# Kernel optimization log

Hardware: AMD Instinct MI355X
Metric: run time of the kernel (lower is better)

Reference implementation:

```python
import jax, jax.numpy as jnp
import numpy as np

B, L, E = 4, 2048, 1024
H, D = 16, 64  # heads, head_dim; H*D == E


def setup_inputs() -> dict:
    key = jax.random.key(0)
    ks = jax.random.split(key, 6)
    s = 0.02
    return {
        "x": jax.random.normal(ks[0], (B, L, E), dtype=jnp.float32),
        "Wq": jax.random.normal(ks[1], (E, H * D), dtype=jnp.float32) * s,
        "Wk": jax.random.normal(ks[2], (E, H * D), dtype=jnp.float32) * s,
        "Wv": jax.random.normal(ks[3], (E, H * D), dtype=jnp.float32) * s,
        "Wo": jax.random.normal(ks[4], (H * D, E), dtype=jnp.float32) * s,
        "bo": jax.random.normal(ks[5], (E,), dtype=jnp.float32) * s,
    }


def reference(x, Wq, Wk, Wv, Wo, bo):
    b, l, e = x.shape
    q = (x @ Wq).reshape(b, l, H, D)
    k = (x @ Wk).reshape(b, l, H, D)
    v = (x @ Wv).reshape(b, l, H, D)
    # NOTE: original scales by sqrt(embed_size), not sqrt(head_dim)
    energy = jnp.einsum('nqhd,nkhd->nhqk', q, k)
    attn = jax.nn.softmax(energy / jnp.sqrt(jnp.float32(e)), axis=3)
    out = jnp.einsum('nhql,nlhd->nqhd', attn, v).reshape(b, l, H * D)
    return out @ Wo + bo
```

## Files before the change

kernel.cpp:

```cpp
#include <hip/hip_runtime.h>

#define B_ 4
#define L_ 2048
#define E_ 1024
#define H_ 16
#define D_ 64
#define CSCALE 0.045084960222629414f

typedef short s16x8 __attribute__((ext_vector_type(8)));
typedef short s16x4 __attribute__((ext_vector_type(4)));
typedef float f32x4 __attribute__((ext_vector_type(4)));

__device__ __forceinline__ unsigned short f2bf(float f) {
  union { float f; unsigned int u; } v;
  v.f = f;
  unsigned int u = v.u;
  u += 0x7fffu + ((u >> 16) & 1u);
  return (unsigned short)(u >> 16);
}

__device__ __forceinline__ void async16(const void* g, void* l) {
  __builtin_amdgcn_global_load_lds(
      (__attribute__((address_space(1))) void*)(g),
      (__attribute__((address_space(3))) void*)(l), 16, 0, 0);
}

__global__ void k_prep(const float* __restrict__ x,
                       const float* __restrict__ Wq, const float* __restrict__ Wk,
                       const float* __restrict__ Wv, const float* __restrict__ Wo,
                       unsigned short* __restrict__ xb,
                       unsigned short* __restrict__ Wt, unsigned short* __restrict__ WoT) {
  __shared__ float t[32][33];
  int bid = blockIdx.x, tid = threadIdx.x;
  if (bid < 8192) {
    int i = bid * 256 + tid;
    float4 v = ((const float4*)x)[i];
    ushort4 o;
    o.x = f2bf(v.x); o.y = f2bf(v.y); o.z = f2bf(v.z); o.w = f2bf(v.w);
    ((ushort4*)xb)[i] = o;
    return;
  }
  int tt = bid - 8192;
  int wsel = tt >> 10, tile = tt & 1023;
  const float* in = (wsel == 0) ? Wq : (wsel == 1) ? Wk : (wsel == 2) ? Wv : Wo;
  unsigned short* out = (wsel == 0) ? Wt : (wsel == 1) ? Wt + (1u << 20)
                        : (wsel == 2) ? Wt + (2u << 20) : WoT;
  int bx = tile & 31, by = tile >> 5;
  int tx = tid & 31, ty = tid >> 5;
  int xcol = bx * 32 + tx;
  int y0 = by * 32;
#pragma unroll
  for (int i = 0; i < 4; ++i)
    t[ty + i * 8][tx] = in[(size_t)(y0 + ty + i * 8) * 1024 + xcol];
  __syncthreads();
  int xo = by * 32 + tx;
  int yo0 = bx * 32;
#pragma unroll
  for (int i = 0; i < 4; ++i)
    out[(size_t)(yo0 + ty + i * 8) * 1024 + xo] = f2bf(t[tx][ty + i * 8]);
}

__global__ __launch_bounds__(256) void k_gemm_qkvt(
    const unsigned short* __restrict__ xb, const unsigned short* __restrict__ Wt,
    unsigned short* __restrict__ Qb, unsigned short* __restrict__ Kb,
    unsigned short* __restrict__ Vt) {
  __shared__ __align__(16) unsigned short As[128 * 32];
  __shared__ __align__(16) unsigned short Bs[128 * 32];
  const int bid = blockIdx.x;
  const int tid = threadIdx.x;
  const int w = tid >> 6, lane = tid & 63;
  const int quad = lane >> 4, mrow = lane & 15;
  const bool isQK = bid < 1024;
  int m0, n0;
  const unsigned short *PA, *PB;
  if (isQK) {
    m0 = (bid & 63) * 128;
    n0 = (bid >> 6) * 128;
    PA = xb + (size_t)m0 * 1024;
    PB = Wt + (size_t)n0 * 1024;
  } else {
    int g = bid - 1024;
    m0 = (g & 7) * 128;
    n0 = (g >> 3) * 128;
    PA = Wt + (2u << 20) + (size_t)m0 * 1024;
    PB = xb + (size_t)n0 * 1024;
  }
  const int wr = (w >> 1) * 64, wc = (w & 1) * 64;
  const f32x4 fz = {0.f, 0.f, 0.f, 0.f};
  f32x4 acc[4][4];
#pragma unroll
  for (int a = 0; a < 4; ++a)
#pragma unroll
    for (int b = 0; b < 4; ++b) acc[a][b] = fz;

  for (int kt = 0; kt < 32; ++kt) {
    __syncthreads();
#pragma unroll
    for (int r = 0; r < 2; ++r) {
      int c = r * 256 + tid;
      int row = c >> 2, cc = c & 3;
      async16(PA + (size_t)row * 1024 + kt * 32 + cc * 8, &As[c * 8]);
    }
#pragma unroll
    for (int r = 0; r < 2; ++r) {
      int c = r * 256 + tid;
      int row = c >> 2, cc = c & 3;
      async16(PB + (size_t)row * 1024 + kt * 32 + cc * 8, &Bs[c * 8]);
    }
    __syncthreads();
    s16x8 a[4], b[4];
#pragma unroll
    for (int mt = 0; mt < 4; ++mt)
      a[mt] = *(const s16x8*)&As[(wr + mt * 16 + mrow) * 32 + quad * 8];
#pragma unroll
    for (int nt = 0; nt < 4; ++nt)
      b[nt] = *(const s16x8*)&Bs[(wc + nt * 16 + mrow) * 32 + quad * 8];
#pragma unroll
    for (int mt = 0; mt < 4; ++mt)
#pragma unroll
      for (int nt = 0; nt < 4; ++nt)
        acc[mt][nt] = __builtin_amdgcn_mfma_f32_16x16x32_bf16(a[mt], b[nt], acc[mt][nt], 0, 0, 0);
  }
  if (isQK) {
#pragma unroll
    for (int mt = 0; mt < 4; ++mt)
#pragma unroll
      for (int nt = 0; nt < 4; ++nt)
#pragma unroll
        for (int i = 0; i < 4; ++i) {
          int row = m0 + wr + mt * 16 + quad * 4 + i;
          int col = n0 + wc + nt * 16 + mrow;
          int bb = row >> 11, l = row & 2047;
          if (col < 1024) {
            int h = col >> 6, d = col & 63;
            Qb[(((size_t)(bb * 16 + h)) * 2048 + l) * 64 + d] = f2bf(acc[mt][nt][i]);
          } else {
            int c2 = col - 1024, h = c2 >> 6, d = c2 & 63;
            Kb[(((size_t)(bb * 16 + h)) * 2048 + l) * 64 + d] = f2bf(acc[mt][nt][i] * CSCALE);
          }
        }
  } else {
#pragma unroll
    for (int mt = 0; mt < 4; ++mt)
#pragma unroll
      for (int nt = 0; nt < 4; ++nt)
#pragma unroll
        for (int i = 0; i < 4; ++i) {
          int f = m0 + wr + mt * 16 + quad * 4 + i;
          int tk = n0 + wc + nt * 16 + mrow;
          int bb = tk >> 11, l = tk & 2047;
          Vt[((size_t)(bb * 1024 + f)) * 2048 + l] = f2bf(acc[mt][nt][i]);
        }
  }
}

__global__ __launch_bounds__(256, 4) void k_attn(
    const unsigned short* __restrict__ Qb, const unsigned short* __restrict__ Kb,
    const unsigned short* __restrict__ Vt, unsigned short* __restrict__ AO) {
  __shared__ __align__(16) unsigned short KVs[2][8192];
  const int tid = threadIdx.x, w = tid >> 6, lane = tid & 63;
  const int quad = lane >> 4, mrow = lane & 15;
  const int bh = blockIdx.y;
  const int q0 = blockIdx.x * 128;
  const unsigned short* Qh = Qb + (size_t)bh * 2048 * 64;
  const unsigned short* Kh = Kb + (size_t)bh * 2048 * 64;
  const unsigned short* Vh = Vt + (size_t)bh * 64 * 2048;
  unsigned short* KVf = &KVs[0][0];

#pragma unroll
  for (int r = 0; r < 4; ++r) {
    int c = r * 256 + tid;
    int row = c >> 3, cl = c & 7;
    int gc = cl ^ (row & 7);
    async16(Qh + (size_t)(q0 + row) * 64 + gc * 8, &KVf[c * 8]);
  }
  __syncthreads();
  s16x8 qb[2][2];
#pragma unroll
  for (int nt = 0; nt < 2; ++nt)
#pragma unroll
    for (int ks = 0; ks < 2; ++ks) {
      int row = w * 32 + nt * 16 + mrow;
      qb[nt][ks] = *(const s16x8*)&KVf[row * 64 + (((ks * 4 + quad) ^ (row & 7)) << 3)];
    }
  __syncthreads();

#pragma unroll
  for (int r = 0; r < 2; ++r) {
    int c = r * 256 + tid;
    int row = c >> 3, cl = c & 7;
    int gc = cl ^ (row & 7);
    async16(Kh + (size_t)row * 64 + gc * 8, &KVs[0][c * 8]);
    async16(Vh + (size_t)row * 2048 + gc * 8, &KVs[0][4096 + c * 8]);
  }

  const f32x4 fz = {0.f, 0.f, 0.f, 0.f};
  f32x4 o[2][4];
  float lr[2];
#pragma unroll
  for (int nt = 0; nt < 2; ++nt) {
    lr[nt] = 0.f;
#pragma unroll
    for (int dt = 0; dt < 4; ++dt) o[nt][dt] = fz;
  }

  for (int j = 0; j < 32; ++j) {
    __syncthreads();
    const unsigned short* Kt = &KVs[j & 1][0];
    const unsigned short* Vs = &KVs[j & 1][4096];

    if (j + 1 < 32) {
      unsigned short* nb = &KVs[(j + 1) & 1][0];
#pragma unroll
      for (int r = 0; r < 2; ++r) {
        int c = r * 256 + tid;
        int row = c >> 3, cl = c & 7;
        int gc = cl ^ (row & 7);
        async16(Kh + (size_t)((j + 1) * 64 + row) * 64 + gc * 8, &nb[c * 8]);
        async16(Vh + (size_t)row * 2048 + (j + 1) * 64 + gc * 8, &nb[4096 + c * 8]);
      }
    }

    s16x4 pa[4][2];
#pragma unroll
    for (int mt = 0; mt < 4; ++mt) {
      int row = mt * 16 + mrow;
      s16x8 ak0 = *(const s16x8*)&Kt[row * 64 + (((0 * 4 + quad) ^ (row & 7)) << 3)];
      s16x8 ak1 = *(const s16x8*)&Kt[row * 64 + (((1 * 4 + quad) ^ (row & 7)) << 3)];
      f32x4 s0 = fz, s1 = fz;
      __builtin_amdgcn_s_setprio(1);
      s0 = __builtin_amdgcn_mfma_f32_16x16x32_bf16(ak0, qb[0][0], s0, 0, 0, 0);
      s1 = __builtin_amdgcn_mfma_f32_16x16x32_bf16(ak0, qb[1][0], s1, 0, 0, 0);
      s0 = __builtin_amdgcn_mfma_f32_16x16x32_bf16(ak1, qb[0][1], s0, 0, 0, 0);
      s1 = __builtin_amdgcn_mfma_f32_16x16x32_bf16(ak1, qb[1][1], s1, 0, 0, 0);
      __builtin_amdgcn_s_setprio(0);
#pragma unroll
      for (int nt = 0; nt < 2; ++nt) {
        const f32x4 sv = nt ? s1 : s0;
        float p0 = __builtin_amdgcn_exp2f(sv[0]);
        float p1 = __builtin_amdgcn_exp2f(sv[1]);
        float p2 = __builtin_amdgcn_exp2f(sv[2]);
        float p3 = __builtin_amdgcn_exp2f(sv[3]);
        lr[nt] += (p0 + p1) + (p2 + p3);
        unsigned int r01, r23;
        asm("v_cvt_pk_bf16_f32 %0, %1, %2" : "=v"(r01) : "v"(p0), "v"(p1));
        asm("v_cvt_pk_bf16_f32 %0, %1, %2" : "=v"(r23) : "v"(p2), "v"(p3));
        union { unsigned int u[2]; s16x4 v4; } uu;
        uu.u[0] = r01; uu.u[1] = r23;
        pa[mt][nt] = uu.v4;
      }
    }

#pragma unroll
    for (int lt = 0; lt < 4; ++lt) {
      s16x4 vb[4];
      int lbase = lt * 16 + quad * 4;
      int cg = lbase >> 3, off = lbase & 7;
#pragma unroll
      for (int dt = 0; dt < 4; ++dt) {
        int row = dt * 16 + mrow;
        vb[dt] = *(const s16x4*)&Vs[row * 64 + ((cg ^ (row & 7)) << 3) + off];
      }
      __builtin_amdgcn_s_setprio(1);
#pragma unroll
      for (int nt = 0; nt < 2; ++nt)
#pragma unroll
        for (int dt = 0; dt < 4; ++dt)
          o[nt][dt] = __builtin_amdgcn_mfma_f32_16x16x16bf16_1k(pa[lt][nt], vb[dt], o[nt][dt], 0, 0, 0);
      __builtin_amdgcn_s_setprio(0);
    }
  }

#pragma unroll
  for (int nt = 0; nt < 2; ++nt) {
    float v = lr[nt];
    v += __shfl_xor(v, 16);
    v += __shfl_xor(v, 32);
    lr[nt] = v;
  }

  int b_ = bh >> 4, h = bh & 15;
#pragma unroll
  for (int nt = 0; nt < 2; ++nt)
#pragma unroll
    for (int i = 0; i < 4; ++i) {
      float inv = 1.f / __shfl(lr[nt], quad * 4 + i, 64);
      int qrow = q0 + w * 32 + nt * 16 + quad * 4 + i;
#pragma unroll
      for (int dt = 0; dt < 4; ++dt) {
        int d = dt * 16 + mrow;
        AO[((size_t)(b_ * 2048 + qrow)) * 1024 + h * 64 + d] = f2bf(o[nt][dt][i] * inv);
      }
    }
}

__global__ __launch_bounds__(256) void k_gemm_out(
    const unsigned short* __restrict__ Ab, const unsigned short* __restrict__ WoT,
    const float* __restrict__ bo, float* __restrict__ out) {
  __shared__ __align__(16) unsigned short As[128 * 32];
  __shared__ __align__(16) unsigned short Bs[128 * 32];
  const int tid = threadIdx.x;
  const int w = tid >> 6, lane = tid & 63;
  const int quad = lane >> 4, mrow = lane & 15;
  const int m0 = blockIdx.x * 128, n0 = blockIdx.y * 128;
  const int wr = (w >> 1) * 64, wc = (w & 1) * 64;
  const f32x4 fz = {0.f, 0.f, 0.f, 0.f};
  f32x4 acc[4][4];
#pragma unroll
  for (int a = 0; a < 4; ++a)
#pragma unroll
    for (int b = 0; b < 4; ++b) acc[a][b] = fz;

  for (int kt = 0; kt < 32; ++kt) {
    __syncthreads();
#pragma unroll
    for (int r = 0; r < 2; ++r) {
      int c = r * 256 + tid;
      int row = c >> 2, cc = c & 3;
      async16(Ab + (size_t)(m0 + row) * 1024 + kt * 32 + cc * 8, &As[c * 8]);
    }
#pragma unroll
    for (int r = 0; r < 2; ++r) {
      int c = r * 256 + tid;
      int row = c >> 2, cc = c & 3;
      async16(WoT + (size_t)(n0 + row) * 1024 + kt * 32 + cc * 8, &Bs[c * 8]);
    }
    __syncthreads();
    s16x8 a[4], b[4];
#pragma unroll
    for (int mt = 0; mt < 4; ++mt)
      a[mt] = *(const s16x8*)&As[(wr + mt * 16 + mrow) * 32 + quad * 8];
#pragma unroll
    for (int nt = 0; nt < 4; ++nt)
      b[nt] = *(const s16x8*)&Bs[(wc + nt * 16 + mrow) * 32 + quad * 8];
#pragma unroll
    for (int mt = 0; mt < 4; ++mt)
#pragma unroll
      for (int nt = 0; nt < 4; ++nt)
        acc[mt][nt] = __builtin_amdgcn_mfma_f32_16x16x32_bf16(a[mt], b[nt], acc[mt][nt], 0, 0, 0);
  }
#pragma unroll
  for (int mt = 0; mt < 4; ++mt)
#pragma unroll
    for (int nt = 0; nt < 4; ++nt)
#pragma unroll
      for (int i = 0; i < 4; ++i) {
        int row = m0 + wr + mt * 16 + quad * 4 + i;
        int col = n0 + wc + nt * 16 + mrow;
        out[(size_t)row * 1024 + col] = acc[mt][nt][i] + bo[col];
      }
}

extern "C" void kernel_launch(void* const* d_in, const int* in_sizes, int n_in,
                              void* d_out, int out_size, void* d_ws, size_t ws_size,
                              hipStream_t stream) {
  const float* x  = (const float*)d_in[0];
  const float* Wq = (const float*)d_in[1];
  const float* Wk = (const float*)d_in[2];
  const float* Wv = (const float*)d_in[3];
  const float* Wo = (const float*)d_in[4];
  const float* bo = (const float*)d_in[5];
  float* out = (float*)d_out;

  char* ws = (char*)d_ws;
  const size_t MiB = 1u << 20;
  unsigned short* xb  = (unsigned short*)(ws);
  unsigned short* Wt  = (unsigned short*)(ws + 16 * MiB);
  unsigned short* WoT = (unsigned short*)(ws + 22 * MiB);
  unsigned short* Qb  = (unsigned short*)(ws + 24 * MiB);
  unsigned short* Kb  = (unsigned short*)(ws + 40 * MiB);
  unsigned short* Vt  = (unsigned short*)(ws + 56 * MiB);
  unsigned short* AO  = xb;

  k_prep<<<12288, 256, 0, stream>>>(x, Wq, Wk, Wv, Wo, xb, Wt, WoT);
  k_gemm_qkvt<<<1536, 256, 0, stream>>>(xb, Wt, Qb, Kb, Vt);
  k_attn<<<dim3(16, 64), 256, 0, stream>>>(Qb, Kb, Vt, AO);
  k_gemm_out<<<dim3(64, 8), 256, 0, stream>>>(AO, WoT, bo, out);
}
```

Before: 276.4 us.

## Enlarge attention blocks, triple-buffer KV tiles, and software-pipeline QK/exp/PV stages

The attention kernel now uses 512-thread blocks covering 256 query rows, halving the grid, with a 4-slot LDS ring that keeps K/V tiles two iterations ahead. Full __syncthreads is replaced by an explicit vmcnt wait plus s_barrier, so only the older loads have to land before each step. The inner loop is reordered so QK MFMAs for later subtiles interleave with exp/pack and PV MFMAs of earlier ones, hiding latency. The cost is twice the LDS per block, which may lower occupancy, and the wrapped prefetch at the end issues redundant loads.

```diff
diff --git a/kernel.cpp b/kernel.cpp
--- a/kernel.cpp
+++ b/kernel.cpp
@@ -154,14 +154,78 @@
   }
 }
 
-__global__ __launch_bounds__(256, 4) void k_attn(
+struct AK { s16x8 k0, k1; };
+struct ST { f32x4 s0, s1; };
+struct PAT { s16x4 n0, n1; };
+
+__device__ __forceinline__ AK load_ak(const unsigned short* Kt, int mt, int mrow, int quad) {
+  int row = mt * 16 + mrow;
+  AK r;
+  r.k0 = *(const s16x8*)&Kt[row * 64 + (((0 + quad) ^ (row & 7)) << 3)];
+  r.k1 = *(const s16x8*)&Kt[row * 64 + (((4 + quad) ^ (row & 7)) << 3)];
+  return r;
+}
+
+__device__ __forceinline__ ST qkmm(const AK& a, const s16x8 (&qb)[2][2]) {
+  const f32x4 fz = {0.f, 0.f, 0.f, 0.f};
+  ST t; t.s0 = fz; t.s1 = fz;
+  __builtin_amdgcn_s_setprio(1);
+  t.s0 = __builtin_amdgcn_mfma_f32_16x16x32_bf16(a.k0, qb[0][0], t.s0, 0, 0, 0);
+  t.s1 = __builtin_amdgcn_mfma_f32_16x16x32_bf16(a.k0, qb[1][0], t.s1, 0, 0, 0);
+  t.s0 = __builtin_amdgcn_mfma_f32_16x16x32_bf16(a.k1, qb[0][1], t.s0, 0, 0, 0);
+  t.s1 = __builtin_amdgcn_mfma_f32_16x16x32_bf16(a.k1, qb[1][1], t.s1, 0, 0, 0);
+  __builtin_amdgcn_s_setprio(0);
+  return t;
+}
+
+__device__ __forceinline__ s16x4 exp_pack(const f32x4 sv, float& lracc) {
+  float p0 = __builtin_amdgcn_exp2f(sv[0]);
+  float p1 = __builtin_amdgcn_exp2f(sv[1]);
+  float p2 = __builtin_amdgcn_exp2f(sv[2]);
+  float p3 = __builtin_amdgcn_exp2f(sv[3]);
+  lracc += (p0 + p1) + (p2 + p3);
+  unsigned int r01, r23;
+  asm("v_cvt_pk_bf16_f32 %0, %1, %2" : "=v"(r01) : "v"(p0), "v"(p1));
+  asm("v_cvt_pk_bf16_f32 %0, %1, %2" : "=v"(r23) : "v"(p2), "v"(p3));
+  union { unsigned int u[2]; s16x4 v4; } uu;
+  uu.u[0] = r01; uu.u[1] = r23;
+  return uu.v4;
+}
+
+__device__ __forceinline__ PAT expp(const ST& t, float (&lr)[2]) {
+  PAT r;
+  r.n0 = exp_pack(t.s0, lr[0]);
+  r.n1 = exp_pack(t.s1, lr[1]);
+  return r;
+}
+
+__device__ __forceinline__ void pv(const unsigned short* Vs, int lt, const PAT& p,
+                                   f32x4 (&o)[2][4], int mrow, int quad) {
+  s16x4 vb[4];
+  int lbase = lt * 16 + quad * 4;
+  int cg = lbase >> 3, off = lbase & 7;
+#pragma unroll
+  for (int dt = 0; dt < 4; ++dt) {
+    int row = dt * 16 + mrow;
+    vb[dt] = *(const s16x4*)&Vs[row * 64 + ((cg ^ (row & 7)) << 3) + off];
+  }
+  __builtin_amdgcn_s_setprio(1);
+#pragma unroll
+  for (int dt = 0; dt < 4; ++dt) {
+    o[0][dt] = __builtin_amdgcn_mfma_f32_16x16x16bf16_1k(p.n0, vb[dt], o[0][dt], 0, 0, 0);
+    o[1][dt] = __builtin_amdgcn_mfma_f32_16x16x16bf16_1k(p.n1, vb[dt], o[1][dt], 0, 0, 0);
+  }
+  __builtin_amdgcn_s_setprio(0);
+}
+
+__global__ __launch_bounds__(512) void k_attn(
     const unsigned short* __restrict__ Qb, const unsigned short* __restrict__ Kb,
     const unsigned short* __restrict__ Vt, unsigned short* __restrict__ AO) {
-  __shared__ __align__(16) unsigned short KVs[2][8192];
+  __shared__ __align__(16) unsigned short KVs[4][8192];
   const int tid = threadIdx.x, w = tid >> 6, lane = tid & 63;
   const int quad = lane >> 4, mrow = lane & 15;
   const int bh = blockIdx.y;
-  const int q0 = blockIdx.x * 128;
+  const int q0 = blockIdx.x * 256;
   const unsigned short* Qh = Qb + (size_t)bh * 2048 * 64;
   const unsigned short* Kh = Kb + (size_t)bh * 2048 * 64;
   const unsigned short* Vh = Vt + (size_t)bh * 64 * 2048;
@@ -169,12 +233,14 @@
 
 #pragma unroll
   for (int r = 0; r < 4; ++r) {
-    int c = r * 256 + tid;
+    int c = r * 512 + tid;
     int row = c >> 3, cl = c & 7;
     int gc = cl ^ (row & 7);
     async16(Qh + (size_t)(q0 + row) * 64 + gc * 8, &KVf[c * 8]);
   }
-  __syncthreads();
+  asm volatile("s_waitcnt vmcnt(0)" ::: "memory");
+  __builtin_amdgcn_s_barrier();
+  asm volatile("" ::: "memory");
   s16x8 qb[2][2];
 #pragma unroll
   for (int nt = 0; nt < 2; ++nt)
@@ -183,15 +249,16 @@
       int row = w * 32 + nt * 16 + mrow;
       qb[nt][ks] = *(const s16x8*)&KVf[row * 64 + (((ks * 4 + quad) ^ (row & 7)) << 3)];
     }
-  __syncthreads();
-
-#pragma unroll
-  for (int r = 0; r < 2; ++r) {
-    int c = r * 256 + tid;
-    int row = c >> 3, cl = c & 7;
-    int gc = cl ^ (row & 7);
-    async16(Kh + (size_t)row * 64 + gc * 8, &KVs[0][c * 8]);
-    async16(Vh + (size_t)row * 2048 + gc * 8, &KVs[0][4096 + c * 8]);
+  asm volatile("" ::: "memory");
+  __builtin_amdgcn_s_barrier();
+  asm volatile("" ::: "memory");
+
+  {
+    int row = tid >> 3, cl = tid & 7, gc = cl ^ (row & 7);
+    async16(Kh + (size_t)row * 64 + gc * 8, &KVs[0][tid * 8]);
+    async16(Vh + (size_t)row * 2048 + gc * 8, &KVs[0][4096 + tid * 8]);
+    async16(Kh + (size_t)(64 + row) * 64 + gc * 8, &KVs[1][tid * 8]);
+    async16(Vh + (size_t)row * 2048 + 64 + gc * 8, &KVs[1][4096 + tid * 8]);
   }
 
   const f32x4 fz = {0.f, 0.f, 0.f, 0.f};
@@ -205,70 +272,31 @@
   }
 
   for (int j = 0; j < 32; ++j) {
-    __syncthreads();
-    const unsigned short* Kt = &KVs[j & 1][0];
-    const unsigned short* Vs = &KVs[j & 1][4096];
-
-    if (j + 1 < 32) {
-      unsigned short* nb = &KVs[(j + 1) & 1][0];
-#pragma unroll
-      for (int r = 0; r < 2; ++r) {
-        int c = r * 256 + tid;
-        int row = c >> 3, cl = c & 7;
-        int gc = cl ^ (row & 7);
-        async16(Kh + (size_t)((j + 1) * 64 + row) * 64 + gc * 8, &nb[c * 8]);
-        async16(Vh + (size_t)row * 2048 + (j + 1) * 64 + gc * 8, &nb[4096 + c * 8]);
-      }
-    }
-
-    s16x4 pa[4][2];
-#pragma unroll
-    for (int mt = 0; mt < 4; ++mt) {
-      int row = mt * 16 + mrow;
-      s16x8 ak0 = *(const s16x8*)&Kt[row * 64 + (((0 * 4 + quad) ^ (row & 7)) << 3)];
-      s16x8 ak1 = *(const s16x8*)&Kt[row * 64 + (((1 * 4 + quad) ^ (row & 7)) << 3)];
-      f32x4 s0 = fz, s1 = fz;
-      __builtin_amdgcn_s_setprio(1);
-      s0 = __builtin_amdgcn_mfma_f32_16x16x32_bf16(ak0, qb[0][0], s0, 0, 0, 0);
-      s1 = __builtin_amdgcn_mfma_f32_16x16x32_bf16(ak0, qb[1][0], s1, 0, 0, 0);
-      s0 = __builtin_amdgcn_mfma_f32_16x16x32_bf16(ak1, qb[0][1], s0, 0, 0, 0);
-      s1 = __builtin_amdgcn_mfma_f32_16x16x32_bf16(ak1, qb[1][1], s1, 0, 0, 0);
-      __builtin_amdgcn_s_setprio(0);
-#pragma unroll
-      for (int nt = 0; nt < 2; ++nt) {
-        const f32x4 sv = nt ? s1 : s0;
-        float p0 = __builtin_amdgcn_exp2f(sv[0]);
-        float p1 = __builtin_amdgcn_exp2f(sv[1]);
-        float p2 = __builtin_amdgcn_exp2f(sv[2]);
-        float p3 = __builtin_amdgcn_exp2f(sv[3]);
-        lr[nt] += (p0 + p1) + (p2 + p3);
-        unsigned int r01, r23;
-        asm("v_cvt_pk_bf16_f32 %0, %1, %2" : "=v"(r01) : "v"(p0), "v"(p1));
-        asm("v_cvt_pk_bf16_f32 %0, %1, %2" : "=v"(r23) : "v"(p2), "v"(p3));
-        union { unsigned int u[2]; s16x4 v4; } uu;
-        uu.u[0] = r01; uu.u[1] = r23;
-        pa[mt][nt] = uu.v4;
-      }
-    }
-
-#pragma unroll
-    for (int lt = 0; lt < 4; ++lt) {
-      s16x4 vb[4];
-      int lbase = lt * 16 + quad * 4;
-      int cg = lbase >> 3, off = lbase & 7;
-#pragma unroll
-      for (int dt = 0; dt < 4; ++dt) {
-        int row = dt * 16 + mrow;
-        vb[dt] = *(const s16x4*)&Vs[row * 64 + ((cg ^ (row & 7)) << 3) + off];
-      }
-      __builtin_amdgcn_s_setprio(1);
-#pragma unroll
-      for (int nt = 0; nt < 2; ++nt)
-#pragma unroll
-        for (int dt = 0; dt < 4; ++dt)
-          o[nt][dt] = __builtin_amdgcn_mfma_f32_16x16x16bf16_1k(pa[lt][nt], vb[dt], o[nt][dt], 0, 0, 0);
-      __builtin_amdgcn_s_setprio(0);
-    }
+    {
+      int jj = (j + 2) & 31;
+      unsigned short* nb = &KVs[(j + 2) & 3][0];
+      int row = tid >> 3, cl = tid & 7, gc = cl ^ (row & 7);
+      async16(Kh + (size_t)(jj * 64 + row) * 64 + gc * 8, &nb[tid * 8]);
+      async16(Vh + (size_t)row * 2048 + jj * 64 + gc * 8, &nb[4096 + tid * 8]);
+    }
+    asm volatile("s_waitcnt vmcnt(4)" ::: "memory");
+    __builtin_amdgcn_s_barrier();
+    asm volatile("" ::: "memory");
+    const unsigned short* Kt = &KVs[j & 3][0];
+    const unsigned short* Vs = &KVs[j & 3][4096];
+
+    AK a0 = load_ak(Kt, 0, mrow, quad); ST t0 = qkmm(a0, qb);
+    AK a1 = load_ak(Kt, 1, mrow, quad); ST t1 = qkmm(a1, qb);
+    PAT p0 = expp(t0, lr);
+    AK a2 = load_ak(Kt, 2, mrow, quad); ST t2 = qkmm(a2, qb);
+    pv(Vs, 0, p0, o, mrow, quad);
+    PAT p1 = expp(t1, lr);
+    AK a3 = load_ak(Kt, 3, mrow, quad); ST t3 = qkmm(a3, qb);
+    pv(Vs, 1, p1, o, mrow, quad);
+    PAT p2 = expp(t2, lr);
+    pv(Vs, 2, p2, o, mrow, quad);
+    PAT p3 = expp(t3, lr);
+    pv(Vs, 3, p3, o, mrow, quad);
   }
 
 #pragma unroll
@@ -374,6 +402,6 @@
 
   k_prep<<<12288, 256, 0, stream>>>(x, Wq, Wk, Wv, Wo, xb, Wt, WoT);
   k_gemm_qkvt<<<1536, 256, 0, stream>>>(xb, Wt, Qb, Kb, Vt);
-  k_attn<<<dim3(16, 64), 256, 0, stream>>>(Qb, Kb, Vt, AO);
+  k_attn<<<dim3(8, 64), 512, 0, stream>>>(Qb, Kb, Vt, AO);
   k_gemm_out<<<dim3(64, 8), 256, 0, stream>>>(AO, WoT, bo, out);
 }
```

Result: no change. 278.3 us (+0.7%).
